# Performance work log

Measured on AMD Instinct MI355X. Metric: run time of the kernel, lower is better.

Reference implementation:

```python
import jax, jax.numpy as jnp
import numpy as np

N = 100000
E = 1600000
IN_C, HID_C, OUT_C = 128, 128, 47


def setup_inputs() -> dict:
    key = jax.random.key(0)
    ks = jax.random.split(key, 10)
    x = jax.random.normal(ks[0], (N, IN_C), dtype=jnp.float32)
    edge_index = jax.random.randint(ks[1], (2, E), 0, N, dtype=jnp.int64)
    edge_attr = jax.random.normal(ks[2], (E, 8), dtype=jnp.float32)
    # GCNConv weights (glorot-like scale) and biases
    W1 = jax.random.normal(ks[3], (IN_C, HID_C), dtype=jnp.float32) / np.sqrt(IN_C)
    b1 = jnp.zeros((HID_C,), dtype=jnp.float32)
    W2 = jax.random.normal(ks[4], (HID_C, HID_C), dtype=jnp.float32) / np.sqrt(HID_C)
    b2 = jnp.zeros((HID_C,), dtype=jnp.float32)
    W3 = jax.random.normal(ks[5], (HID_C, OUT_C), dtype=jnp.float32) / np.sqrt(HID_C)
    b3 = jnp.zeros((OUT_C,), dtype=jnp.float32)
    return {"x": x, "edge_index": edge_index, "edge_attr": edge_attr,
            "W1": W1, "b1": b1, "W2": W2, "b2": b2, "W3": W3, "b3": b3}


def _gcn_norm(edge_index, num_nodes):
    # GCNConv default: add self-loops, symmetric normalization D^-1/2 (A+I) D^-1/2
    row, col = edge_index[0], edge_index[1]
    deg = jax.ops.segment_sum(jnp.ones((edge_index.shape[1],), jnp.float32), row,
                              num_segments=num_nodes) + 1.0  # +1 for self-loop
    dis = jax.lax.rsqrt(deg)  # deg >= 1, always finite
    edge_norm = dis[row] * dis[col]   # [E]
    self_norm = dis * dis             # [N], self-loop weight
    return edge_norm, self_norm


def _gcn_conv(h, W, b, row, col, edge_norm, self_norm, num_nodes):
    h = h @ W                                  # linear transform first (PyG order)
    msg = edge_norm[:, None] * h[col]          # [E, C] gathered, normalized messages
    agg = jax.ops.segment_sum(msg, row, num_segments=num_nodes)
    return agg + self_norm[:, None] * h + b    # self-loop contribution + bias


def reference(x, edge_index, edge_attr, W1, b1, W2, b2, W3, b3):
    # edge_attr is accepted but unused, matching the original forward.
    row, col = edge_index[0], edge_index[1]
    edge_norm, self_norm = _gcn_norm(edge_index, N)
    # layer 1 + relu (dropout is identity in eval mode)
    h = _gcn_conv(x, W1, b1, row, col, edge_norm, self_norm, N)
    h = jax.nn.relu(h)
    # layer 2 + relu
    h = _gcn_conv(h, W2, b2, row, col, edge_norm, self_norm, N)
    h = jax.nn.relu(h)
    # final layer, no activation
    return _gcn_conv(h, W3, b3, row, col, edge_norm, self_norm, N)
```

## Files before the change

### kernel.cpp

```cpp
#include <hip/hip_runtime.h>
#include <hip/hip_fp16.h>
#include <cstdint>
#include <cstddef>

#define N_NODES 100000
#define N_EDGES 1600000
#define BSHIFT 9
#define BSIZE (1 << BSHIFT)
#define NB ((N_NODES + BSIZE - 1) >> BSHIFT)
#define PTILE 4096

typedef _Float16 half8 __attribute__((ext_vector_type(8)));
typedef float floatx4 __attribute__((ext_vector_type(4)));
typedef int v4i __attribute__((ext_vector_type(4)));

__device__ float llvm_amdgcn_raw_buffer_load_fp32(v4i srsrc, int voffset,
                                                  int soffset, int aux)
    __asm("llvm.amdgcn.raw.buffer.load.f32");

static __device__ __forceinline__ v4i make_srsrc(const void* p) {
    unsigned long long a = (unsigned long long)p;
    v4i r;
    r[0] = (int)(unsigned)(a & 0xFFFFFFFFull);
    r[1] = (int)(unsigned)((a >> 32) & 0xFFFFull);
    r[2] = -1;
    r[3] = 0x00020000;
    return r;
}

static __device__ __forceinline__ __half2 f_as_h2(float f) {
    union { float f; __half2 h; } u; u.f = f; return u.h;
}

static __device__ __forceinline__ int edge_row(const void* ei, int i64, int e) {
    return i64 ? (int)((const long long*)ei)[e] : ((const int*)ei)[e];
}
static __device__ __forceinline__ int edge_col(const void* ei, int i64, int e) {
    return i64 ? (int)((const long long*)ei)[N_EDGES + e] : ((const int*)ei)[N_EDGES + e];
}

__global__ void detect_i64(const int* __restrict__ w, int* __restrict__ flag) {
    __shared__ int red[256];
    int acc = 0;
    for (int j = threadIdx.x; j < 2048; j += 256) {
        int k = j * 781;
        acc |= w[2 * k + 1];
    }
    red[threadIdx.x] = acc;
    __syncthreads();
    for (int off = 128; off > 0; off >>= 1) {
        if (threadIdx.x < off) red[threadIdx.x] |= red[threadIdx.x + off];
        __syncthreads();
    }
    if (threadIdx.x == 0) *flag = (red[0] == 0) ? 1 : 0;
}

__global__ void init_pre(int* __restrict__ bsize) {
    if (threadIdx.x < NB + 1) bsize[threadIdx.x] = 0;
}

__global__ void __launch_bounds__(256)
hist_buckets(const void* __restrict__ ei, const int* __restrict__ flag,
             int* __restrict__ bsize) {
    __shared__ int h[256];
    const int tid = threadIdx.x;
    const int tbase = blockIdx.x * PTILE;
    const int f = *flag;
    h[tid] = 0;
    __syncthreads();
    #pragma unroll
    for (int j = 0; j < PTILE / 256; ++j) {
        int idx = tbase + tid + j * 256;
        if (idx < N_EDGES) {
            int r = edge_row(ei, f, idx);
            atomicAdd(&h[r >> BSHIFT], 1);
        }
    }
    __syncthreads();
    if (tid < NB && h[tid] > 0) atomicAdd(&bsize[tid], h[tid]);
}

__global__ void scan_buckets(const int* __restrict__ bsize, int* __restrict__ bbase,
                             int* __restrict__ bcur) {
    __shared__ int sd[256];
    int t = threadIdx.x;
    int v = (t < NB) ? bsize[t] : 0;
    sd[t] = v;
    __syncthreads();
    for (int off = 1; off < 256; off <<= 1) {
        int add = (t >= off) ? sd[t - off] : 0;
        __syncthreads();
        sd[t] += add;
        __syncthreads();
    }
    if (t < NB) {
        bbase[t] = sd[t] - v;
        bcur[t] = sd[t] - v;
    }
    if (t == 255) bbase[NB] = sd[255];
}

__global__ void __launch_bounds__(256)
partition_edges(const void* __restrict__ ei, const int* __restrict__ flag,
                int* __restrict__ bcur, int* __restrict__ bktRow,
                int* __restrict__ bktCol) {
    __shared__ int rows[PTILE];
    __shared__ int cols[PTILE];
    __shared__ int h[256], sc[256], exs[256], base_s[256], p[256];

    const int tid = threadIdx.x;
    const int tbase = blockIdx.x * PTILE;
    const int tot = min(PTILE, N_EDGES - tbase);
    const int f = *flag;

    h[tid] = 0;
    p[tid] = 0;
    __syncthreads();

    #pragma unroll
    for (int j = 0; j < PTILE / 256; ++j) {
        int idx = tbase + tid + j * 256;
        if (idx < N_EDGES) {
            int r = edge_row(ei, f, idx);
            atomicAdd(&h[r >> BSHIFT], 1);
        }
    }
    __syncthreads();

    sc[tid] = h[tid];
    __syncthreads();
    for (int off = 1; off < 256; off <<= 1) {
        int v = (tid >= off) ? sc[tid - off] : 0;
        __syncthreads();
        sc[tid] += v;
        __syncthreads();
    }
    exs[tid] = sc[tid] - h[tid];
    if (tid < NB && h[tid] > 0) base_s[tid] = atomicAdd(&bcur[tid], h[tid]);
    __syncthreads();

    #pragma unroll
    for (int j = 0; j < PTILE / 256; ++j) {
        int idx = tbase + tid + j * 256;
        if (idx < N_EDGES) {
            int r = edge_row(ei, f, idx);
            int c = edge_col(ei, f, idx);
            int b = r >> BSHIFT;
            int lp = atomicAdd(&p[b], 1);
            int slot = exs[b] + lp;
            rows[slot] = r;
            cols[slot] = c;
        }
    }
    __syncthreads();

    for (int slot = tid; slot < tot; slot += 256) {
        int r = rows[slot];
        int b = r >> BSHIFT;
        int addr = base_s[b] + (slot - exs[b]);
        bktRow[addr] = r;
        bktCol[addr] = cols[slot];
    }
}

__global__ void __launch_bounds__(512)
bucket_stats(const int* __restrict__ bktRow, const int* __restrict__ bbase,
             int* __restrict__ deg, int* __restrict__ rowst) {
    __shared__ int cnt[512];
    __shared__ int sd[512];
    const int b = blockIdx.x;
    const int t = threadIdx.x;
    const int start = bbase[b], end = bbase[b + 1];
    cnt[t] = 0;
    __syncthreads();
    for (int i = start + t; i < end; i += 512)
        atomicAdd(&cnt[bktRow[i] - (b << BSHIFT)], 1);
    __syncthreads();
    int v = cnt[t];
    sd[t] = v;
    __syncthreads();
    for (int off = 1; off < 512; off <<= 1) {
        int add = (t >= off) ? sd[t - off] : 0;
        __syncthreads();
        sd[t] += add;
        __syncthreads();
    }
    int node = (b << BSHIFT) + t;
    if (node < N_NODES) {
        deg[node] = v;
        rowst[node] = start + sd[t] - v;
    }
}

__global__ void compute_dis(const int* __restrict__ deg, float* __restrict__ dis) {
    int i = blockIdx.x * blockDim.x + threadIdx.x;
    if (i < N_NODES) dis[i] = rsqrtf((float)deg[i] + 1.0f);
}

__global__ void __launch_bounds__(512)
scatter_bucket(const int* __restrict__ bktRow, const int* __restrict__ bktCol,
               const int* __restrict__ bbase, const int* __restrict__ rowst,
               const float* __restrict__ dis, int2* __restrict__ csr_cn) {
    __shared__ int cur[512];
    __shared__ float dl[512];
    const int b = blockIdx.x;
    const int t = threadIdx.x;
    const int start = bbase[b], end = bbase[b + 1];
    int node = (b << BSHIFT) + t;
    cur[t] = (node < N_NODES) ? rowst[node] : 0;
    dl[t]  = (node < N_NODES) ? dis[node] : 0.f;
    __syncthreads();
    for (int i = start + t; i < end; i += 512) {
        int r = bktRow[i];
        int c = bktCol[i];
        int lr = r - (b << BSHIFT);
        int pos = atomicAdd(&cur[lr], 1);
        float nrm = dl[lr] * dis[c];
        csr_cn[pos] = make_int2(c, __float_as_int(nrm));
    }
}

template<typename TIn, int NT>
__global__ void __launch_bounds__(256)
gemm_mfma(const TIn* __restrict__ in, const float* __restrict__ W,
          __half* __restrict__ out, int Mfull) {
    constexpr int NCOL = NT * 16;
    __shared__ _Float16 Wt[NCOL * 128];

    const int tid = threadIdx.x;
    for (int chunkIdx = tid; chunkIdx < NCOL * 16; chunkIdx += 256) {
        int n = chunkIdx % NCOL;
        int c = chunkIdx / NCOL;
        half8 v;
        #pragma unroll
        for (int i = 0; i < 8; ++i) {
            int k = c * 8 + i;
            v[i] = (n < Mfull) ? (_Float16)W[k * Mfull + n] : (_Float16)0.f;
        }
        *(half8*)&Wt[n * 128 + (c ^ (n & 7)) * 8] = v;
    }
    __syncthreads();

    const int wave = tid >> 6, lane = tid & 63;
    const int quad = lane >> 4, m = lane & 15;
    const int rowbase = blockIdx.x * 64 + wave * 16;
    const int arow_i = rowbase + m;
    const bool avalid = arow_i < N_NODES;
    const TIn* arow = in + (size_t)(avalid ? arow_i : 0) * 128;

    half8 a[4];
    #pragma unroll
    for (int kt = 0; kt < 4; ++kt) {
        if constexpr (sizeof(TIn) == 4) {
            const float4* ptr = (const float4*)((const float*)arow + kt * 32 + quad * 8);
            float4 f0 = ptr[0];
            float4 f1 = ptr[1];
            a[kt][0] = (_Float16)f0.x; a[kt][1] = (_Float16)f0.y;
            a[kt][2] = (_Float16)f0.z; a[kt][3] = (_Float16)f0.w;
            a[kt][4] = (_Float16)f1.x; a[kt][5] = (_Float16)f1.y;
            a[kt][6] = (_Float16)f1.z; a[kt][7] = (_Float16)f1.w;
        } else {
            a[kt] = *(const half8*)((const _Float16*)arow + kt * 32 + quad * 8);
        }
    }

    floatx4 acc[NT];
    #pragma unroll
    for (int ct = 0; ct < NT; ++ct) acc[ct] = (floatx4){0.f, 0.f, 0.f, 0.f};

    #pragma unroll
    for (int ct = 0; ct < NT; ++ct) {
        #pragma unroll
        for (int kt = 0; kt < 4; ++kt) {
            int n = ct * 16 + m;
            half8 bfrag = *(const half8*)&Wt[n * 128 + ((kt * 4 + quad) ^ (m & 7)) * 8];
            acc[ct] = __builtin_amdgcn_mfma_f32_16x16x32_f16(a[kt], bfrag, acc[ct], 0, 0, 0);
        }
    }

    const int rs0 = rowbase + quad * 4;
    #pragma unroll
    for (int ct = 0; ct < NT; ++ct) {
        int col = ct * 16 + m;
        if (col >= Mfull) continue;
        #pragma unroll
        for (int r = 0; r < 4; ++r) {
            int rs = rs0 + r;
            if (rs < N_NODES)
                out[(size_t)rs * Mfull + col] = __float2half(acc[ct][r]);
        }
    }
}

#define AGG_DEPTH 6
#define AGG_BLOCKS 2048

__global__ void __launch_bounds__(256)
agg_c128(const __half* __restrict__ t, const int* __restrict__ rowst,
         const int* __restrict__ deg, const int2* __restrict__ cn,
         const float* __restrict__ dis, const float* __restrict__ bias,
         __half* __restrict__ out, int relu) {
    const int gwave = blockIdx.x * (blockDim.x >> 6) + (threadIdx.x >> 6);
    const int nw = gridDim.x * (blockDim.x >> 6);
    const int lane = threadIdx.x & 63;
    const float2 bv = ((const float2*)bias)[lane];
    const v4i trsrc = make_srsrc(t);
    const int voff_lane = lane << 2;

    for (int w = gwave; w < N_NODES; w += nw) {
        int s = rowst[w], d = deg[w];
        float di = dis[w];
        float sn = di * di;
        float2 tv = __half22float2(((const __half2*)(t + (size_t)w * 128))[lane]);
        float ax = fmaf(sn, tv.x, bv.x);
        float ay = fmaf(sn, tv.y, bv.y);
        int e = s + d;
        int j = s;
        if (j + AGG_DEPTH <= e) {
            int2 c[AGG_DEPTH];
            #pragma unroll
            for (int q = 0; q < AGG_DEPTH; ++q) c[q] = cn[j + q];
            j += AGG_DEPTH;
            while (j + AGG_DEPTH <= e) {
                int2 n[AGG_DEPTH];
                #pragma unroll
                for (int q = 0; q < AGG_DEPTH; ++q) n[q] = cn[j + q];
                __half2 v[AGG_DEPTH];
                #pragma unroll
                for (int q = 0; q < AGG_DEPTH; ++q)
                    v[q] = f_as_h2(llvm_amdgcn_raw_buffer_load_fp32(
                        trsrc, (c[q].x << 8) | voff_lane, 0, 1));
                #pragma unroll
                for (int q = 0; q < AGG_DEPTH; ++q) {
                    float2 fv = __half22float2(v[q]);
                    float nw2 = __int_as_float(c[q].y);
                    ax = fmaf(nw2, fv.x, ax);
                    ay = fmaf(nw2, fv.y, ay);
                }
                #pragma unroll
                for (int q = 0; q < AGG_DEPTH; ++q) c[q] = n[q];
                j += AGG_DEPTH;
            }
            #pragma unroll
            for (int q = 0; q < AGG_DEPTH; ++q) {
                __half2 vv = f_as_h2(llvm_amdgcn_raw_buffer_load_fp32(
                    trsrc, (c[q].x << 8) | voff_lane, 0, 1));
                float2 fv = __half22float2(vv);
                float nw2 = __int_as_float(c[q].y);
                ax = fmaf(nw2, fv.x, ax);
                ay = fmaf(nw2, fv.y, ay);
            }
        }
        for (; j < e; ++j) {
            int2 c = cn[j];
            __half2 vv = f_as_h2(llvm_amdgcn_raw_buffer_load_fp32(
                trsrc, (c.x << 8) | voff_lane, 0, 1));
            float2 fv = __half22float2(vv);
            float nw2 = __int_as_float(c.y);
            ax = fmaf(nw2, fv.x, ax);
            ay = fmaf(nw2, fv.y, ay);
        }
        if (relu) { ax = fmaxf(ax, 0.f); ay = fmaxf(ay, 0.f); }
        ((__half2*)(out + (size_t)w * 128))[lane] = __float22half2_rn(make_float2(ax, ay));
    }
}

__global__ void __launch_bounds__(256)
agg_c47(const __half* __restrict__ t, const int* __restrict__ rowst,
        const int* __restrict__ deg, const int2* __restrict__ cn,
        const float* __restrict__ dis, const float* __restrict__ bias,
        float* __restrict__ out) {
    const int gwave = blockIdx.x * (blockDim.x >> 6) + (threadIdx.x >> 6);
    const int nw = gridDim.x * (blockDim.x >> 6);
    const int lane = threadIdx.x & 63;
    const bool act = lane < 47;
    const int li = act ? lane : 0;
    const float bvs = bias[li];

    for (int w = gwave; w < N_NODES; w += nw) {
        int s = rowst[w], d = deg[w];
        float di = dis[w];
        float sn = di * di;
        float acc = act ? fmaf(sn, (float)t[(size_t)w * 47 + li], bvs) : 0.f;
        int e = s + d;
        int j = s;
        if (j + AGG_DEPTH <= e) {
            int2 c[AGG_DEPTH];
            #pragma unroll
            for (int q = 0; q < AGG_DEPTH; ++q) c[q] = cn[j + q];
            j += AGG_DEPTH;
            while (j + AGG_DEPTH <= e) {
                int2 n[AGG_DEPTH];
                #pragma unroll
                for (int q = 0; q < AGG_DEPTH; ++q) n[q] = cn[j + q];
                __half v[AGG_DEPTH];
                #pragma unroll
                for (int q = 0; q < AGG_DEPTH; ++q)
                    v[q] = t[(size_t)c[q].x * 47 + li];
                #pragma unroll
                for (int q = 0; q < AGG_DEPTH; ++q)
                    acc = fmaf(__int_as_float(c[q].y), (float)v[q], acc);
                #pragma unroll
                for (int q = 0; q < AGG_DEPTH; ++q) c[q] = n[q];
                j += AGG_DEPTH;
            }
            #pragma unroll
            for (int q = 0; q < AGG_DEPTH; ++q)
                acc = fmaf(__int_as_float(c[q].y), (float)t[(size_t)c[q].x * 47 + li], acc);
        }
        for (; j < e; ++j) {
            int2 c = cn[j];
            acc = fmaf(__int_as_float(c.y), (float)t[(size_t)c.x * 47 + li], acc);
        }
        if (act) out[(size_t)w * 47 + lane] = acc;
    }
}

extern "C" void kernel_launch(void* const* d_in, const int* in_sizes, int n_in,
                              void* d_out, int out_size, void* d_ws, size_t ws_size,
                              hipStream_t stream) {
    const float* x  = (const float*)d_in[0];
    const void*  ei = d_in[1];
    const float* W1 = (const float*)d_in[3];
    const float* b1 = (const float*)d_in[4];
    const float* W2 = (const float*)d_in[5];
    const float* b2 = (const float*)d_in[6];
    const float* W3 = (const float*)d_in[7];
    const float* b3 = (const float*)d_in[8];
    float* out = (float*)d_out;

    size_t off = 0;
    auto alloc = [&](size_t bytes) -> void* {
        void* p = (char*)d_ws + off;
        off += (bytes + 511) & ~(size_t)511;
        return p;
    };
    float*  dis     = (float*)alloc((size_t)N_NODES * 4);
    int*    deg     = (int*)  alloc((size_t)N_NODES * 4);
    int*    rowst   = (int*)  alloc((size_t)N_NODES * 4);
    int*    bsize   = (int*)  alloc((NB + 1) * 4);
    int*    bbase   = (int*)  alloc((NB + 1) * 4);
    int*    bcur    = (int*)  alloc(NB * 4);
    int*    flag    = (int*)  alloc(64);
    int2*   csr_cn  = (int2*) alloc((size_t)N_EDGES * 8);
    __half* tbuf    = (__half*)alloc((size_t)N_NODES * 128 * 2);
    __half* hbuf    = (__half*)alloc((size_t)N_NODES * 128 * 2);
    int*    bktRow  = (int*)hbuf;
    int*    bktCol  = bktRow + N_EDGES;
    (void)ws_size; (void)in_sizes; (void)n_in; (void)out_size;

    int ptiles = (N_EDGES + PTILE - 1) / PTILE;

    detect_i64<<<1, 256, 0, stream>>>((const int*)ei, flag);
    init_pre<<<1, 256, 0, stream>>>(bsize);
    hist_buckets<<<ptiles, 256, 0, stream>>>(ei, flag, bsize);
    scan_buckets<<<1, 256, 0, stream>>>(bsize, bbase, bcur);
    partition_edges<<<ptiles, 256, 0, stream>>>(ei, flag, bcur, bktRow, bktCol);
    bucket_stats<<<NB, 512, 0, stream>>>(bktRow, bbase, deg, rowst);
    compute_dis<<<(N_NODES + 255) / 256, 256, 0, stream>>>(deg, dis);
    scatter_bucket<<<NB, 512, 0, stream>>>(bktRow, bktCol, bbase, rowst, dis, csr_cn);

    int gblocks = (N_NODES + 63) / 64;

    gemm_mfma<float, 8><<<gblocks, 256, 0, stream>>>(x, W1, tbuf, 128);
    agg_c128<<<AGG_BLOCKS, 256, 0, stream>>>(tbuf, rowst, deg, csr_cn, dis, b1, hbuf, 1);
    gemm_mfma<_Float16, 8><<<gblocks, 256, 0, stream>>>((_Float16*)hbuf, W2, tbuf, 128);
    agg_c128<<<AGG_BLOCKS, 256, 0, stream>>>(tbuf, rowst, deg, csr_cn, dis, b2, hbuf, 1);
    gemm_mfma<_Float16, 3><<<gblocks, 256, 0, stream>>>((_Float16*)hbuf, W3, tbuf, 47);
    agg_c47<<<AGG_BLOCKS, 256, 0, stream>>>(tbuf, rowst, deg, csr_cn, dis, b3, out);
}
```

Before: 509.6 us.

## Pad final-layer features to stride 64 and split edges across half-waves

The last GEMM now writes its 47-column output with a row stride of 64, so each row is 128-byte aligned. The 47-channel aggregation is reworked so each half-wave loads half2 pairs and processes alternating edges, then the two halves combine with a cross-lane shuffle; before, 17 of 64 lanes sat idle on scalar half loads. Separately, the bucket-size init is merged into the int64-detect kernel and the rsqrt degree normalization is folded into bucket_stats, removing two small launches. The padded columns are never written, but they are only read into lanes whose results are discarded.

```diff
diff --git a/kernel.cpp b/kernel.cpp
--- a/kernel.cpp
+++ b/kernel.cpp
@@ -39,24 +39,24 @@
     return i64 ? (int)((const long long*)ei)[N_EDGES + e] : ((const int*)ei)[N_EDGES + e];
 }
 
-__global__ void detect_i64(const int* __restrict__ w, int* __restrict__ flag) {
-    __shared__ int red[256];
+__global__ void __launch_bounds__(1024)
+detect_i64(const int* __restrict__ w, int* __restrict__ flag,
+           int* __restrict__ bsize) {
+    __shared__ int red[1024];
+    const int tid = threadIdx.x;
+    if (tid < NB + 1) bsize[tid] = 0;
     int acc = 0;
-    for (int j = threadIdx.x; j < 2048; j += 256) {
+    for (int j = tid; j < 2048; j += 1024) {
         int k = j * 781;
         acc |= w[2 * k + 1];
     }
-    red[threadIdx.x] = acc;
-    __syncthreads();
-    for (int off = 128; off > 0; off >>= 1) {
-        if (threadIdx.x < off) red[threadIdx.x] |= red[threadIdx.x + off];
-        __syncthreads();
-    }
-    if (threadIdx.x == 0) *flag = (red[0] == 0) ? 1 : 0;
-}
-
-__global__ void init_pre(int* __restrict__ bsize) {
-    if (threadIdx.x < NB + 1) bsize[threadIdx.x] = 0;
+    red[tid] = acc;
+    __syncthreads();
+    for (int off = 512; off > 0; off >>= 1) {
+        if (tid < off) red[tid] |= red[tid + off];
+        __syncthreads();
+    }
+    if (tid == 0) *flag = (red[0] == 0) ? 1 : 0;
 }
 
 __global__ void __launch_bounds__(256)
@@ -165,7 +165,8 @@
 
 __global__ void __launch_bounds__(512)
 bucket_stats(const int* __restrict__ bktRow, const int* __restrict__ bbase,
-             int* __restrict__ deg, int* __restrict__ rowst) {
+             int* __restrict__ deg, int* __restrict__ rowst,
+             float* __restrict__ dis) {
     __shared__ int cnt[512];
     __shared__ int sd[512];
     const int b = blockIdx.x;
@@ -189,12 +190,8 @@
     if (node < N_NODES) {
         deg[node] = v;
         rowst[node] = start + sd[t] - v;
-    }
-}
-
-__global__ void compute_dis(const int* __restrict__ deg, float* __restrict__ dis) {
-    int i = blockIdx.x * blockDim.x + threadIdx.x;
-    if (i < N_NODES) dis[i] = rsqrtf((float)deg[i] + 1.0f);
+        dis[node] = rsqrtf((float)v + 1.0f);
+    }
 }
 
 __global__ void __launch_bounds__(512)
@@ -223,7 +220,7 @@
 template<typename TIn, int NT>
 __global__ void __launch_bounds__(256)
 gemm_mfma(const TIn* __restrict__ in, const float* __restrict__ W,
-          __half* __restrict__ out, int Mfull) {
+          __half* __restrict__ out, int Mfull, int ostride) {
     constexpr int NCOL = NT * 16;
     __shared__ _Float16 Wt[NCOL * 128];
 
@@ -287,7 +284,7 @@
         for (int r = 0; r < 4; ++r) {
             int rs = rs0 + r;
             if (rs < N_NODES)
-                out[(size_t)rs * Mfull + col] = __float2half(acc[ct][r]);
+                out[(size_t)rs * ostride + col] = __float2half(acc[ct][r]);
         }
     }
 }
@@ -365,6 +362,8 @@
     }
 }
 
+#define C47_DEPTH 4
+
 __global__ void __launch_bounds__(256)
 agg_c47(const __half* __restrict__ t, const int* __restrict__ rowst,
         const int* __restrict__ deg, const int2* __restrict__ cn,
@@ -373,46 +372,67 @@
     const int gwave = blockIdx.x * (blockDim.x >> 6) + (threadIdx.x >> 6);
     const int nw = gridDim.x * (blockDim.x >> 6);
     const int lane = threadIdx.x & 63;
-    const bool act = lane < 47;
-    const int li = act ? lane : 0;
-    const float bvs = bias[li];
+    const int hw = lane >> 5;
+    const int l2 = lane & 31;
+    const int ch0 = l2 * 2, ch1 = ch0 + 1;
+    const float b0 = (ch0 < 47) ? bias[ch0] : 0.f;
+    const float b1 = (ch1 < 47) ? bias[ch1] : 0.f;
 
     for (int w = gwave; w < N_NODES; w += nw) {
         int s = rowst[w], d = deg[w];
         float di = dis[w];
         float sn = di * di;
-        float acc = act ? fmaf(sn, (float)t[(size_t)w * 47 + li], bvs) : 0.f;
+        float2 tv = __half22float2(((const __half2*)(t + (size_t)w * 64))[l2]);
+        float ax = (hw == 0) ? sn * tv.x : 0.f;
+        float ay = (hw == 0) ? sn * tv.y : 0.f;
         int e = s + d;
-        int j = s;
-        if (j + AGG_DEPTH <= e) {
-            int2 c[AGG_DEPTH];
+        int j = s + hw;
+        if (j + 2 * C47_DEPTH <= e + 1) {
+            int2 c[C47_DEPTH];
             #pragma unroll
-            for (int q = 0; q < AGG_DEPTH; ++q) c[q] = cn[j + q];
-            j += AGG_DEPTH;
-            while (j + AGG_DEPTH <= e) {
-                int2 n[AGG_DEPTH];
-                #pragma unroll
-                for (int q = 0; q < AGG_DEPTH; ++q) n[q] = cn[j + q];
-                __half v[AGG_DEPTH];
-                #pragma unroll
-                for (int q = 0; q < AGG_DEPTH; ++q)
-                    v[q] = t[(size_t)c[q].x * 47 + li];
-                #pragma unroll
-                for (int q = 0; q < AGG_DEPTH; ++q)
-                    acc = fmaf(__int_as_float(c[q].y), (float)v[q], acc);
-                #pragma unroll
-                for (int q = 0; q < AGG_DEPTH; ++q) c[q] = n[q];
-                j += AGG_DEPTH;
+            for (int q = 0; q < C47_DEPTH; ++q) c[q] = cn[j + 2 * q];
+            j += 2 * C47_DEPTH;
+            while (j + 2 * C47_DEPTH <= e + 1) {
+                int2 n[C47_DEPTH];
+                #pragma unroll
+                for (int q = 0; q < C47_DEPTH; ++q) n[q] = cn[j + 2 * q];
+                __half2 v[C47_DEPTH];
+                #pragma unroll
+                for (int q = 0; q < C47_DEPTH; ++q)
+                    v[q] = ((const __half2*)(t + (size_t)c[q].x * 64))[l2];
+                #pragma unroll
+                for (int q = 0; q < C47_DEPTH; ++q) {
+                    float2 fv = __half22float2(v[q]);
+                    float nw2 = __int_as_float(c[q].y);
+                    ax = fmaf(nw2, fv.x, ax);
+                    ay = fmaf(nw2, fv.y, ay);
+                }
+                #pragma unroll
+                for (int q = 0; q < C47_DEPTH; ++q) c[q] = n[q];
+                j += 2 * C47_DEPTH;
             }
             #pragma unroll
-            for (int q = 0; q < AGG_DEPTH; ++q)
-                acc = fmaf(__int_as_float(c[q].y), (float)t[(size_t)c[q].x * 47 + li], acc);
-        }
-        for (; j < e; ++j) {
+            for (int q = 0; q < C47_DEPTH; ++q) {
+                __half2 vv = ((const __half2*)(t + (size_t)c[q].x * 64))[l2];
+                float2 fv = __half22float2(vv);
+                float nw2 = __int_as_float(c[q].y);
+                ax = fmaf(nw2, fv.x, ax);
+                ay = fmaf(nw2, fv.y, ay);
+            }
+        }
+        for (; j < e; j += 2) {
             int2 c = cn[j];
-            acc = fmaf(__int_as_float(c.y), (float)t[(size_t)c.x * 47 + li], acc);
-        }
-        if (act) out[(size_t)w * 47 + lane] = acc;
+            float2 fv = __half22float2(((const __half2*)(t + (size_t)c.x * 64))[l2]);
+            float nw2 = __int_as_float(c.y);
+            ax = fmaf(nw2, fv.x, ax);
+            ay = fmaf(nw2, fv.y, ay);
+        }
+        ax += __shfl_xor(ax, 32);
+        ay += __shfl_xor(ay, 32);
+        if (hw == 0) {
+            if (ch0 < 47) out[(size_t)w * 47 + ch0] = ax + b0;
+            if (ch1 < 47) out[(size_t)w * 47 + ch1] = ay + b1;
+        }
     }
 }
 
@@ -451,21 +471,19 @@
 
     int ptiles = (N_EDGES + PTILE - 1) / PTILE;
 
-    detect_i64<<<1, 256, 0, stream>>>((const int*)ei, flag);
-    init_pre<<<1, 256, 0, stream>>>(bsize);
+    detect_i64<<<1, 1024, 0, stream>>>((const int*)ei, flag, bsize);
     hist_buckets<<<ptiles, 256, 0, stream>>>(ei, flag, bsize);
     scan_buckets<<<1, 256, 0, stream>>>(bsize, bbase, bcur);
     partition_edges<<<ptiles, 256, 0, stream>>>(ei, flag, bcur, bktRow, bktCol);
-    bucket_stats<<<NB, 512, 0, stream>>>(bktRow, bbase, deg, rowst);
-    compute_dis<<<(N_NODES + 255) / 256, 256, 0, stream>>>(deg, dis);
+    bucket_stats<<<NB, 512, 0, stream>>>(bktRow, bbase, deg, rowst, dis);
     scatter_bucket<<<NB, 512, 0, stream>>>(bktRow, bktCol, bbase, rowst, dis, csr_cn);
 
     int gblocks = (N_NODES + 63) / 64;
 
-    gemm_mfma<float, 8><<<gblocks, 256, 0, stream>>>(x, W1, tbuf, 128);
+    gemm_mfma<float, 8><<<gblocks, 256, 0, stream>>>(x, W1, tbuf, 128, 128);
     agg_c128<<<AGG_BLOCKS, 256, 0, stream>>>(tbuf, rowst, deg, csr_cn, dis, b1, hbuf, 1);
-    gemm_mfma<_Float16, 8><<<gblocks, 256, 0, stream>>>((_Float16*)hbuf, W2, tbuf, 128);
+    gemm_mfma<_Float16, 8><<<gblocks, 256, 0, stream>>>((_Float16*)hbuf, W2, tbuf, 128, 128);
     agg_c128<<<AGG_BLOCKS, 256, 0, stream>>>(tbuf, rowst, deg, csr_cn, dis, b2, hbuf, 1);
-    gemm_mfma<_Float16, 3><<<gblocks, 256, 0, stream>>>((_Float16*)hbuf, W3, tbuf, 47);
+    gemm_mfma<_Float16, 3><<<gblocks, 256, 0, stream>>>((_Float16*)hbuf, W3, tbuf, 47, 64);
     agg_c47<<<AGG_BLOCKS, 256, 0, stream>>>(tbuf, rowst, deg, csr_cn, dis, b3, out);
 }
```

Measured after the change: 495.3 us (median of 2 runs). 2.8% less time.
